# Optimization experiments

Hardware: AMD Instinct MI355X
Metric: run time of the kernel (lower is better)

Reference implementation:

```python
import jax, jax.numpy as jnp
import numpy as np

N_NODES = 100000
N_EDGES = 1600000
IN_DIM, HID, OUT_DIM = 128, 128, 64


def _glorot(key, fan_in, fan_out):
    s = float(np.sqrt(6.0 / (fan_in + fan_out)))
    return jax.random.uniform(key, (fan_in, fan_out), jnp.float32, -s, s)


def setup_inputs() -> dict:
    key = jax.random.key(0)
    ks = jax.random.split(key, 6)
    x = jax.random.normal(ks[0], (N_NODES, IN_DIM), jnp.float32)
    edge_index = jax.random.randint(ks[1], (2, N_EDGES), 0, N_NODES, jnp.int32)
    return {
        "x": x,
        "edge_index": edge_index,
        "W0": _glorot(ks[2], IN_DIM, HID), "b0": jnp.zeros((HID,), jnp.float32),
        "W1": _glorot(ks[3], HID, HID),    "b1": jnp.zeros((HID,), jnp.float32),
        "W2": _glorot(ks[4], HID, OUT_DIM), "b2": jnp.zeros((OUT_DIM,), jnp.float32),
    }


def _gcn_conv(x, src, dst, norm, W, b):
    # x' = D^{-1/2} (A+I) D^{-1/2} X W + b  (PyG GCNConv, add_self_loops=True)
    h = x @ W                       # [N, F_out]
    msg = h[src] * norm[:, None]    # [E+N, F_out] gathered, normalized messages
    out = jax.ops.segment_sum(msg, dst, num_segments=x.shape[0])
    return out + b


def reference(x, edge_index, W0, b0, W1, b1, W2, b2):
    n = x.shape[0]
    loop = jnp.arange(n, dtype=edge_index.dtype)
    src = jnp.concatenate([edge_index[0], loop])  # self-loops appended
    dst = jnp.concatenate([edge_index[1], loop])
    deg = jax.ops.segment_sum(jnp.ones_like(src, jnp.float32), dst, num_segments=n)
    dis = jnp.where(deg > 0, jax.lax.rsqrt(jnp.maximum(deg, 1e-12)), 0.0)
    norm = dis[src] * dis[dst]      # symmetric GCN normalization per edge

    h = jax.nn.relu(_gcn_conv(x, src, dst, norm, W0, b0))
    h = jax.nn.relu(_gcn_conv(h, src, dst, norm, W1, b1))
    h = jax.nn.relu(_gcn_conv(h, src, dst, norm, W2, b2))
    return jax.nn.log_softmax(h, axis=1)
```

## Files before the change

kernel.cpp:

```cpp
#include <hip/hip_runtime.h>

#define NN 100000
#define NE 1600000
#define NBK 782
#define NBLK 256
#define CHUNK ((NE + NBLK - 1) / NBLK)

typedef __bf16 bf16x4 __attribute__((ext_vector_type(4)));
typedef __bf16 bf16x8 __attribute__((ext_vector_type(8)));
typedef float f32x2 __attribute__((ext_vector_type(2)));
typedef float f32x4 __attribute__((ext_vector_type(4)));

#define ACC8_FP8(vv)                                                                  \
  {                                                                                   \
    f32x2 p;                                                                          \
    p = __builtin_amdgcn_cvt_pk_f32_fp8((vv).x, 0); acc[0] += p[0]; acc[1] += p[1];   \
    p = __builtin_amdgcn_cvt_pk_f32_fp8((vv).x, 1); acc[2] += p[0]; acc[3] += p[1];   \
    p = __builtin_amdgcn_cvt_pk_f32_fp8((vv).y, 0); acc[4] += p[0]; acc[5] += p[1];   \
    p = __builtin_amdgcn_cvt_pk_f32_fp8((vv).y, 1); acc[6] += p[0]; acc[7] += p[1];   \
  }


__global__ __launch_bounds__(256) void k1_hist(const int* __restrict__ dst, int* __restrict__ bhist,
                                               const float* __restrict__ W0, const float* __restrict__ W1,
                                               const float* __restrict__ W2, __bf16* __restrict__ Wt) {
  int b = blockIdx.x;
  if (b >= NBLK) {
    int i = (b - NBLK) * 256 + threadIdx.x;
    if (i < 16384) {
      int k = i >> 7, n = i & 127;
      Wt[n * 128 + k] = (__bf16)W0[i];
    } else if (i < 32768) {
      int j = i - 16384;
      int k = j >> 7, n = j & 127;
      Wt[16384 + n * 128 + k] = (__bf16)W1[j];
    } else if (i < 40960) {
      int j = i - 32768;
      int k = j >> 6, n = j & 63;
      Wt[32768 + n * 128 + k] = (__bf16)W2[j];
    }
    return;
  }
  __shared__ int h[NBK];
  int tid = threadIdx.x;
  for (int i = tid; i < NBK; i += 256) h[i] = 0;
  __syncthreads();
  int base = b * CHUNK, end = min(base + CHUNK, NE);
  for (int e = base + tid; e < end; e += 256) atomicAdd(&h[dst[e] >> 7], 1);
  __syncthreads();
  for (int i = tid; i < NBK; i += 256) bhist[i * NBLK + b] = h[i];
}

__global__ __launch_bounds__(256) void kA2(const int* __restrict__ bhist, int* __restrict__ btot) {
  int w = threadIdx.x >> 6, lane = threadIdx.x & 63;
  int bin = blockIdx.x * 4 + w;
  if (bin >= NBK) return;
  int4 v = *(const int4*)(bhist + bin * NBLK + lane * 4);
  int s = v.x + v.y + v.z + v.w;
#pragma unroll
  for (int off = 32; off > 0; off >>= 1) s += __shfl_xor(s, off);
  if (lane == 0) btot[bin] = s;
}

__global__ __launch_bounds__(1024) void kB_bscan(const int* __restrict__ btot, int* __restrict__ bptr) {
  __shared__ int ws[16];
  int tid = threadIdx.x, lane = tid & 63, w = tid >> 6;
  int v = (tid < NBK) ? btot[tid] : 0;
  int incl = v;
#pragma unroll
  for (int off = 1; off < 64; off <<= 1) {
    int t = __shfl_up(incl, off);
    if (lane >= off) incl += t;
  }
  if (lane == 63) ws[w] = incl;
  __syncthreads();
  if (tid < 16) {
    int s = ws[tid];
    int si = s;
#pragma unroll
    for (int off = 1; off < 16; off <<= 1) {
      int t = __shfl_up(si, off);
      if (lane >= off) si += t;
    }
    ws[tid] = si - s;
  }
  __syncthreads();
  if (tid < NBK) bptr[tid + 1] = incl + ws[w];
  if (tid == 0) bptr[0] = 0;
}

__global__ __launch_bounds__(256) void kC2(const int* __restrict__ bhist, const int* __restrict__ bptr,
                                           int* __restrict__ blockbase) {
  int w = threadIdx.x >> 6, lane = threadIdx.x & 63;
  int bin = blockIdx.x * 4 + w;
  if (bin >= NBK) return;
  int4 v = *(const int4*)(bhist + bin * NBLK + lane * 4);
  int ls = v.x + v.y + v.z + v.w;
  int incl = ls;
#pragma unroll
  for (int off = 1; off < 64; off <<= 1) {
    int t = __shfl_up(incl, off);
    if (lane >= off) incl += t;
  }
  int base = bptr[bin] + incl - ls;
  int4 o;
  o.x = base;
  o.y = base + v.x;
  o.z = base + v.x + v.y;
  o.w = base + v.x + v.y + v.z;
  *(int4*)(blockbase + bin * NBLK + lane * 4) = o;
}

__global__ __launch_bounds__(256) void k3_scatter(const int* __restrict__ src, const int* __restrict__ dst,
                                                  const int* __restrict__ blockbase, int* __restrict__ bucketed) {
  __shared__ int cur[NBK];
  int tid = threadIdx.x, b = blockIdx.x;
  for (int i = tid; i < NBK; i += 256) cur[i] = blockbase[i * NBLK + b];
  __syncthreads();
  int base = b * CHUNK, end = min(base + CHUNK, NE);
  for (int e = base + tid; e < end; e += 256) {
    int d = dst[e];
    int pos = atomicAdd(&cur[d >> 7], 1);
    bucketed[pos] = (src[e] << 7) | (d & 127);
  }
}

__global__ __launch_bounds__(256) void k_degfill(const int* __restrict__ bucketed, const int* __restrict__ bptr,
                                                 int* __restrict__ row_ptr, float* __restrict__ dis,
                                                 int* __restrict__ csr_src) {
  __shared__ int deg[128];
  __shared__ int sc[128];
  __shared__ int cur[128];
  int b = blockIdx.x, tid = threadIdx.x;
  int nb0 = b << 7;
  if (tid < 128) deg[tid] = 0;
  __syncthreads();
  int beg = bptr[b], end = bptr[b + 1];
  for (int e = beg + tid; e < end; e += 256) atomicAdd(&deg[bucketed[e] & 127], 1);
  __syncthreads();
  if (tid < 128) sc[tid] = deg[tid];
  __syncthreads();
  for (int off = 1; off < 128; off <<= 1) {
    int t = (tid >= off && tid < 128) ? sc[tid - off] : 0;
    __syncthreads();
    if (tid < 128) sc[tid] += t;
    __syncthreads();
  }
  if (tid < 128) {
    cur[tid] = beg + sc[tid] - deg[tid];
    if (nb0 + tid < NN) {
      row_ptr[nb0 + tid + 1] = beg + sc[tid];
      dis[nb0 + tid] = rsqrtf((float)(deg[tid] + 1));
      if (b == 0 && tid == 0) row_ptr[0] = 0;
    }
  }
  __syncthreads();
  for (int e = beg + tid; e < end; e += 256) {
    int pk = bucketed[e];
    int pos = atomicAdd(&cur[pk & 127], 1);
    csr_src[pos] = pk >> 7;
  }
}


template <int BN, int MODE, bool OUT8>
__global__ __launch_bounds__(512) void k_gemm(const void* __restrict__ Av, const __bf16* __restrict__ Wt,
                                              const float* __restrict__ bias, const float* __restrict__ dis,
                                              void* __restrict__ outv) {
  constexpr int LDK = 136;
  constexpr int NT = BN / 32;
  constexpr int ROWB = BN * (OUT8 ? 1 : 2);
  __shared__ __bf16 lB[BN * LDK];

  const int tid = threadIdx.x;
  const int rowBase = blockIdx.x * 128;
  const int lane = tid & 63;
  const int wid = tid >> 6;
  const int wm = (wid & 3) * 32;
  const int wn = (wid >> 2) * (BN / 2);
  const int lm = lane & 15;
  const int kg = lane >> 4;

  if (blockIdx.x == 0 && tid < ROWB / 16) {
    ((uint4*)((char*)outv + (size_t)NN * ROWB))[tid] = make_uint4(0, 0, 0, 0);
  }

  for (int c = tid; c < 16 * BN; c += 512) {
    int n = c >> 4;
    int koff = (c & 15) * 8;
    bf16x8 w = *(const bf16x8*)(Wt + n * 128 + koff);
    *(bf16x8*)&lB[n * LDK + koff] = w;
  }
  __syncthreads();

  f32x4 acc[2][NT] = {};
  const bool full = (rowBase + 128 <= NN);

#pragma unroll 2
  for (int ks = 0; ks < 128; ks += 32) {
    int k0 = ks + kg * 8;
    bf16x8 af[2];
    if constexpr (MODE == 0) {
      const float* A = (const float*)Av;
#pragma unroll
      for (int tm = 0; tm < 2; ++tm) {
        int gr = rowBase + wm + tm * 16 + lm;
        f32x4 a0 = {}, a1 = {};
        if (full || gr < NN) {
          a0 = *(const f32x4*)(A + (size_t)gr * 128 + k0);
          a1 = *(const f32x4*)(A + (size_t)gr * 128 + k0 + 4);
        }
        af[tm] = bf16x8{(__bf16)a0[0], (__bf16)a0[1], (__bf16)a0[2], (__bf16)a0[3],
                        (__bf16)a1[0], (__bf16)a1[1], (__bf16)a1[2], (__bf16)a1[3]};
      }
    } else {
      const __bf16* A = (const __bf16*)Av;
      f32x4 b0 = *(const f32x4*)(bias + k0);
      f32x4 b1 = *(const f32x4*)(bias + k0 + 4);
#pragma unroll
      for (int tm = 0; tm < 2; ++tm) {
        int gr = rowBase + wm + tm * 16 + lm;
        bf16x8 v = {};
        if (full || gr < NN) v = *(const bf16x8*)(A + (size_t)gr * 128 + k0);
        af[tm] = bf16x8{(__bf16)fmaxf((float)v[0] + b0[0], 0.f), (__bf16)fmaxf((float)v[1] + b0[1], 0.f),
                        (__bf16)fmaxf((float)v[2] + b0[2], 0.f), (__bf16)fmaxf((float)v[3] + b0[3], 0.f),
                        (__bf16)fmaxf((float)v[4] + b1[0], 0.f), (__bf16)fmaxf((float)v[5] + b1[1], 0.f),
                        (__bf16)fmaxf((float)v[6] + b1[2], 0.f), (__bf16)fmaxf((float)v[7] + b1[3], 0.f)};
      }
    }
    bf16x8 bfr[NT];
#pragma unroll
    for (int tn = 0; tn < NT; ++tn)
      bfr[tn] = *(const bf16x8*)&lB[(wn + tn * 16 + lm) * LDK + k0];
#pragma unroll
    for (int tm = 0; tm < 2; ++tm)
#pragma unroll
      for (int tn = 0; tn < NT; ++tn)
        acc[tm][tn] = __builtin_amdgcn_mfma_f32_16x16x32_bf16(af[tm], bfr[tn], acc[tm][tn], 0, 0, 0);
  }

#pragma unroll
  for (int tm = 0; tm < 2; ++tm) {
    int r0 = rowBase + wm + tm * 16 + kg * 4;
#pragma unroll
    for (int tn = 0; tn < NT; ++tn) {
      int c0 = wn + tn * 16 + lm;
#pragma unroll
      for (int r = 0; r < 4; ++r) {
        int gr = r0 + r;
        if (full || gr < NN) {
          float val = acc[tm][tn][r] * dis[gr];
          if constexpr (OUT8) {
            unsigned char* o8 = (unsigned char*)outv;
            unsigned pk = __builtin_amdgcn_cvt_pk_fp8_f32(val, val, 0, 0);
            o8[(size_t)gr * BN + c0] = (unsigned char)(pk & 0xffu);
          } else {
            __bf16* ob = (__bf16*)outv;
            ob[(size_t)gr * BN + c0] = (__bf16)val;
          }
        }
      }
    }
  }
}


__global__ __launch_bounds__(256) void k_agg128(const unsigned char* __restrict__ tmp8, const int* __restrict__ row_ptr,
                                                const int* __restrict__ csr_src, const float* __restrict__ dis,
                                                __bf16* __restrict__ agg) {
  int qw = (blockIdx.x * 256 + threadIdx.x) >> 6;
  int lane = threadIdx.x & 63;
  int g = lane >> 4;
  int fl = lane & 15;
  int node = qw * 4 + g;

  int beg = row_ptr[node];
  int end = row_ptr[node + 1];

  int mx = end - beg;
  mx = max(mx, __shfl_xor(mx, 16));
  mx = max(mx, __shfl_xor(mx, 32));

  float acc[8] = {};
  {
    uint2 sv = *(const uint2*)(tmp8 + (size_t)node * 128 + fl * 8);
    ACC8_FP8(sv);
  }

  for (int done = 0; done < mx; done += 16) {
    int ep = beg + done + fl;
    int sidx = (ep < end) ? csr_src[ep] : NN;
    int rem = mx - done;
    {
      uint2 v[8];
#pragma unroll
      for (int u = 0; u < 8; ++u) {
        int s = __shfl(sidx, g * 16 + u);
        v[u] = *(const uint2*)(tmp8 + (size_t)s * 128 + fl * 8);
      }
#pragma unroll
      for (int u = 0; u < 8; ++u) ACC8_FP8(v[u]);
    }
    if (rem > 8) {
      uint2 v[8];
#pragma unroll
      for (int u = 0; u < 8; ++u) {
        int s = __shfl(sidx, g * 16 + 8 + u);
        v[u] = *(const uint2*)(tmp8 + (size_t)s * 128 + fl * 8);
      }
#pragma unroll
      for (int u = 0; u < 8; ++u) ACC8_FP8(v[u]);
    }
  }

  float d = dis[node];
  bf16x8 o;
#pragma unroll
  for (int t = 0; t < 8; ++t) o[t] = (__bf16)(acc[t] * d);
  *(bf16x8*)&agg[(size_t)node * 128 + fl * 8] = o;
}


__global__ __launch_bounds__(256) void k_agg64_final(const __bf16* __restrict__ tmp, const int* __restrict__ row_ptr,
                                                     const int* __restrict__ csr_src, const float* __restrict__ dis,
                                                     const float* __restrict__ b2, float* __restrict__ out) {
  int qw = (blockIdx.x * 256 + threadIdx.x) >> 6;
  int lane = threadIdx.x & 63;
  int g = lane >> 4;
  int fl = lane & 15;
  int node = qw * 4 + g;

  int beg = row_ptr[node];
  int end = row_ptr[node + 1];

  int mx = end - beg;
  mx = max(mx, __shfl_xor(mx, 16));
  mx = max(mx, __shfl_xor(mx, 32));

  float acc[4] = {};
  {
    bf16x4 sv = *(const bf16x4*)&tmp[(size_t)node * 64 + fl * 4];
#pragma unroll
    for (int t = 0; t < 4; ++t) acc[t] = (float)sv[t];
  }

  for (int done = 0; done < mx; done += 16) {
    int ep = beg + done + fl;
    int sidx = (ep < end) ? csr_src[ep] : NN;
    int rem = mx - done;
    {
      bf16x4 v[8];
#pragma unroll
      for (int u = 0; u < 8; ++u) {
        int s = __shfl(sidx, g * 16 + u);
        v[u] = *(const bf16x4*)&tmp[(size_t)s * 64 + fl * 4];
      }
#pragma unroll
      for (int u = 0; u < 8; ++u)
#pragma unroll
        for (int t = 0; t < 4; ++t) acc[t] += (float)v[u][t];
    }
    if (rem > 8) {
      bf16x4 v[8];
#pragma unroll
      for (int u = 0; u < 8; ++u) {
        int s = __shfl(sidx, g * 16 + 8 + u);
        v[u] = *(const bf16x4*)&tmp[(size_t)s * 64 + fl * 4];
      }
#pragma unroll
      for (int u = 0; u < 8; ++u)
#pragma unroll
        for (int t = 0; t < 4; ++t) acc[t] += (float)v[u][t];
    }
  }

  float d = dis[node];
  float v4[4], lm = -1e30f;
#pragma unroll
  for (int t = 0; t < 4; ++t) {
    v4[t] = fmaxf(acc[t] * d + b2[fl * 4 + t], 0.f);
    lm = fmaxf(lm, v4[t]);
  }
#pragma unroll
  for (int off = 8; off > 0; off >>= 1) lm = fmaxf(lm, __shfl_xor(lm, off));
  float le = 0.f;
#pragma unroll
  for (int t = 0; t < 4; ++t) le += __expf(v4[t] - lm);
#pragma unroll
  for (int off = 8; off > 0; off >>= 1) le += __shfl_xor(le, off);
  float ls = lm + __logf(le);
  f32x4 o = {v4[0] - ls, v4[1] - ls, v4[2] - ls, v4[3] - ls};
  *(f32x4*)&out[(size_t)node * 64 + fl * 4] = o;
}


extern "C" void kernel_launch(void* const* d_in, const int* in_sizes, int n_in,
                              void* d_out, int out_size, void* d_ws, size_t ws_size,
                              hipStream_t stream) {
  const float* x  = (const float*)d_in[0];
  const int*   ei = (const int*)d_in[1];
  const float* W0 = (const float*)d_in[2];
  const float* b0 = (const float*)d_in[3];
  const float* W1 = (const float*)d_in[4];
  const float* b1 = (const float*)d_in[5];
  const float* W2 = (const float*)d_in[6];
  const float* b2 = (const float*)d_in[7];
  const int* esrc = ei;
  const int* edst = ei + NE;

  char* p = (char*)d_ws;
  auto alloc = [&](size_t bytes) {
    char* q = p;
    p += (bytes + 255) & ~(size_t)255;
    return q;
  };
  float*  dis     = (float*)alloc((size_t)NN * 4);
  int*    row_ptr = (int*)alloc((size_t)(NN + 1) * 4);
  int*    btot    = (int*)alloc(NBK * 4);
  int*    bptr    = (int*)alloc((NBK + 1) * 4);
  __bf16* Wt      = (__bf16*)alloc(40960 * 2);
  int*    csr_src = (int*)alloc((size_t)NE * 4);
  char*   tmp     = (char*)alloc((size_t)(NN + 1) * 128 * 2);
  unsigned char* tmp8 = (unsigned char*)tmp;
  __bf16* tmp16   = (__bf16*)tmp;
  int*    bucketed  = (int*)tmp;
  int*    bhist     = csr_src;
  int*    blockbase = csr_src + NBLK * NBK;

  k1_hist<<<NBLK + 160, 256, 0, stream>>>(edst, bhist, W0, W1, W2, Wt);
  kA2<<<(NBK + 3) / 4, 256, 0, stream>>>(bhist, btot);
  kB_bscan<<<1, 1024, 0, stream>>>(btot, bptr);
  kC2<<<(NBK + 3) / 4, 256, 0, stream>>>(bhist, bptr, blockbase);
  k3_scatter<<<NBLK, 256, 0, stream>>>(esrc, edst, blockbase, bucketed);
  k_degfill<<<NBK, 256, 0, stream>>>(bucketed, bptr, row_ptr, dis, csr_src);

  int gblocks = (NN + 127) / 128;
  int ablocks = NN / 16;

  k_gemm<128, 0, true><<<gblocks, 512, 0, stream>>>(x, Wt, nullptr, dis, tmp8);
  k_agg128<<<ablocks, 256, 0, stream>>>(tmp8, row_ptr, csr_src, dis, (__bf16*)d_out);

  k_gemm<128, 2, true><<<gblocks, 512, 0, stream>>>(d_out, Wt + 16384, b0, dis, tmp8);
  k_agg128<<<ablocks, 256, 0, stream>>>(tmp8, row_ptr, csr_src, dis, (__bf16*)d_out);

  k_gemm<64, 2, false><<<gblocks, 512, 0, stream>>>(d_out, Wt + 32768, b1, dis, tmp16);
  k_agg64_final<<<ablocks, 256, 0, stream>>>(tmp16, row_ptr, csr_src, dis, b2, (float*)d_out);
}
```

Baseline: 319.9 us.

## Make GEMM kernels persistent over row tiles and preload full A rows

New measurement: 339.5 us. 1.06x slower.

```diff
diff --git a/kernel.cpp b/kernel.cpp
--- a/kernel.cpp
+++ b/kernel.cpp
@@ -170,10 +170,10 @@
   constexpr int LDK = 136;
   constexpr int NT = BN / 32;
   constexpr int ROWB = BN * (OUT8 ? 1 : 2);
+  constexpr int NTILE = (NN + 127) / 128;
   __shared__ __bf16 lB[BN * LDK];
 
   const int tid = threadIdx.x;
-  const int rowBase = blockIdx.x * 128;
   const int lane = tid & 63;
   const int wid = tid >> 6;
   const int wm = (wid & 3) * 32;
@@ -188,75 +188,92 @@
   for (int c = tid; c < 16 * BN; c += 512) {
     int n = c >> 4;
     int koff = (c & 15) * 8;
-    bf16x8 w = *(const bf16x8*)(Wt + n * 128 + koff);
-    *(bf16x8*)&lB[n * LDK + koff] = w;
-  }
-  __syncthreads();
-
-  f32x4 acc[2][NT] = {};
-  const bool full = (rowBase + 128 <= NN);
-
-#pragma unroll 2
-  for (int ks = 0; ks < 128; ks += 32) {
-    int k0 = ks + kg * 8;
-    bf16x8 af[2];
-    if constexpr (MODE == 0) {
-      const float* A = (const float*)Av;
+    *(bf16x8*)&lB[n * LDK + koff] = *(const bf16x8*)(Wt + n * 128 + koff);
+  }
+  __syncthreads();
+
+  for (int tile = blockIdx.x; tile < NTILE; tile += 256) {
+    const int rowBase = tile * 128;
+    const bool full = (rowBase + 128 <= NN);
+
+    f32x4 a0[4][2], a1[4][2];
+    bf16x8 araw[4][2];
+#pragma unroll
+    for (int ks4 = 0; ks4 < 4; ++ks4) {
+      int k0 = ks4 * 32 + kg * 8;
 #pragma unroll
       for (int tm = 0; tm < 2; ++tm) {
         int gr = rowBase + wm + tm * 16 + lm;
-        f32x4 a0 = {}, a1 = {};
-        if (full || gr < NN) {
-          a0 = *(const f32x4*)(A + (size_t)gr * 128 + k0);
-          a1 = *(const f32x4*)(A + (size_t)gr * 128 + k0 + 4);
+        if constexpr (MODE == 0) {
+          const float* A = (const float*)Av;
+          a0[ks4][tm] = f32x4{};
+          a1[ks4][tm] = f32x4{};
+          if (full || gr < NN) {
+            a0[ks4][tm] = *(const f32x4*)(A + (size_t)gr * 128 + k0);
+            a1[ks4][tm] = *(const f32x4*)(A + (size_t)gr * 128 + k0 + 4);
+          }
+        } else {
+          const __bf16* A = (const __bf16*)Av;
+          araw[ks4][tm] = bf16x8{};
+          if (full || gr < NN) araw[ks4][tm] = *(const bf16x8*)(A + (size_t)gr * 128 + k0);
         }
-        af[tm] = bf16x8{(__bf16)a0[0], (__bf16)a0[1], (__bf16)a0[2], (__bf16)a0[3],
-                        (__bf16)a1[0], (__bf16)a1[1], (__bf16)a1[2], (__bf16)a1[3]};
-      }
-    } else {
-      const __bf16* A = (const __bf16*)Av;
-      f32x4 b0 = *(const f32x4*)(bias + k0);
-      f32x4 b1 = *(const f32x4*)(bias + k0 + 4);
-#pragma unroll
-      for (int tm = 0; tm < 2; ++tm) {
-        int gr = rowBase + wm + tm * 16 + lm;
-        bf16x8 v = {};
-        if (full || gr < NN) v = *(const bf16x8*)(A + (size_t)gr * 128 + k0);
-        af[tm] = bf16x8{(__bf16)fmaxf((float)v[0] + b0[0], 0.f), (__bf16)fmaxf((float)v[1] + b0[1], 0.f),
-                        (__bf16)fmaxf((float)v[2] + b0[2], 0.f), (__bf16)fmaxf((float)v[3] + b0[3], 0.f),
-                        (__bf16)fmaxf((float)v[4] + b1[0], 0.f), (__bf16)fmaxf((float)v[5] + b1[1], 0.f),
-                        (__bf16)fmaxf((float)v[6] + b1[2], 0.f), (__bf16)fmaxf((float)v[7] + b1[3], 0.f)};
-      }
-    }
-    bf16x8 bfr[NT];
-#pragma unroll
-    for (int tn = 0; tn < NT; ++tn)
-      bfr[tn] = *(const bf16x8*)&lB[(wn + tn * 16 + lm) * LDK + k0];
-#pragma unroll
-    for (int tm = 0; tm < 2; ++tm)
+      }
+    }
+
+    f32x4 acc[2][NT] = {};
+#pragma unroll
+    for (int ks4 = 0; ks4 < 4; ++ks4) {
+      int k0 = ks4 * 32 + kg * 8;
+      bf16x8 af[2];
+      if constexpr (MODE == 0) {
+#pragma unroll
+        for (int tm = 0; tm < 2; ++tm) {
+          f32x4 A0 = a0[ks4][tm], A1 = a1[ks4][tm];
+          af[tm] = bf16x8{(__bf16)A0[0], (__bf16)A0[1], (__bf16)A0[2], (__bf16)A0[3],
+                          (__bf16)A1[0], (__bf16)A1[1], (__bf16)A1[2], (__bf16)A1[3]};
+        }
+      } else {
+        f32x4 b0 = *(const f32x4*)(bias + k0);
+        f32x4 b1 = *(const f32x4*)(bias + k0 + 4);
+#pragma unroll
+        for (int tm = 0; tm < 2; ++tm) {
+          bf16x8 v = araw[ks4][tm];
+          af[tm] = bf16x8{(__bf16)fmaxf((float)v[0] + b0[0], 0.f), (__bf16)fmaxf((float)v[1] + b0[1], 0.f),
+                          (__bf16)fmaxf((float)v[2] + b0[2], 0.f), (__bf16)fmaxf((float)v[3] + b0[3], 0.f),
+                          (__bf16)fmaxf((float)v[4] + b1[0], 0.f), (__bf16)fmaxf((float)v[5] + b1[1], 0.f),
+                          (__bf16)fmaxf((float)v[6] + b1[2], 0.f), (__bf16)fmaxf((float)v[7] + b1[3], 0.f)};
+        }
+      }
+      bf16x8 bfr[NT];
 #pragma unroll
       for (int tn = 0; tn < NT; ++tn)
-        acc[tm][tn] = __builtin_amdgcn_mfma_f32_16x16x32_bf16(af[tm], bfr[tn], acc[tm][tn], 0, 0, 0);
-  }
-
-#pragma unroll
-  for (int tm = 0; tm < 2; ++tm) {
-    int r0 = rowBase + wm + tm * 16 + kg * 4;
-#pragma unroll
-    for (int tn = 0; tn < NT; ++tn) {
-      int c0 = wn + tn * 16 + lm;
-#pragma unroll
-      for (int r = 0; r < 4; ++r) {
-        int gr = r0 + r;
-        if (full || gr < NN) {
-          float val = acc[tm][tn][r] * dis[gr];
-          if constexpr (OUT8) {
-            unsigned char* o8 = (unsigned char*)outv;
-            unsigned pk = __builtin_amdgcn_cvt_pk_fp8_f32(val, val, 0, 0);
-            o8[(size_t)gr * BN + c0] = (unsigned char)(pk & 0xffu);
-          } else {
-            __bf16* ob = (__bf16*)outv;
-            ob[(size_t)gr * BN + c0] = (__bf16)val;
+        bfr[tn] = *(const bf16x8*)&lB[(wn + tn * 16 + lm) * LDK + k0];
+#pragma unroll
+      for (int tm = 0; tm < 2; ++tm)
+#pragma unroll
+        for (int tn = 0; tn < NT; ++tn)
+          acc[tm][tn] = __builtin_amdgcn_mfma_f32_16x16x32_bf16(af[tm], bfr[tn], acc[tm][tn], 0, 0, 0);
+    }
+
+#pragma unroll
+    for (int tm = 0; tm < 2; ++tm) {
+      int r0 = rowBase + wm + tm * 16 + kg * 4;
+#pragma unroll
+      for (int tn = 0; tn < NT; ++tn) {
+        int c0 = wn + tn * 16 + lm;
+#pragma unroll
+        for (int r = 0; r < 4; ++r) {
+          int gr = r0 + r;
+          if (full || gr < NN) {
+            float val = acc[tm][tn][r] * dis[gr];
+            if constexpr (OUT8) {
+              unsigned char* o8 = (unsigned char*)outv;
+              unsigned pk = __builtin_amdgcn_cvt_pk_fp8_f32(val, val, 0, 0);
+              o8[(size_t)gr * BN + c0] = (unsigned char)(pk & 0xffu);
+            } else {
+              __bf16* ob = (__bf16*)outv;
+              ob[(size_t)gr * BN + c0] = (__bf16)val;
+            }
           }
         }
       }
@@ -434,15 +451,14 @@
   k3_scatter<<<NBLK, 256, 0, stream>>>(esrc, edst, blockbase, bucketed);
   k_degfill<<<NBK, 256, 0, stream>>>(bucketed, bptr, row_ptr, dis, csr_src);
 
-  int gblocks = (NN + 127) / 128;
   int ablocks = NN / 16;
 
-  k_gemm<128, 0, true><<<gblocks, 512, 0, stream>>>(x, Wt, nullptr, dis, tmp8);
+  k_gemm<128, 0, true><<<256, 512, 0, stream>>>(x, Wt, nullptr, dis, tmp8);
   k_agg128<<<ablocks, 256, 0, stream>>>(tmp8, row_ptr, csr_src, dis, (__bf16*)d_out);
 
-  k_gemm<128, 2, true><<<gblocks, 512, 0, stream>>>(d_out, Wt + 16384, b0, dis, tmp8);
+  k_gemm<128, 2, true><<<256, 512, 0, stream>>>(d_out, Wt + 16384, b0, dis, tmp8);
   k_agg128<<<ablocks, 256, 0, stream>>>(tmp8, row_ptr, csr_src, dis, (__bf16*)d_out);
 
-  k_gemm<64, 2, false><<<gblocks, 512, 0, stream>>>(d_out, Wt + 32768, b1, dis, tmp16);
+  k_gemm<64, 2, false><<<256, 512, 0, stream>>>(d_out, Wt + 32768, b1, dis, tmp16);
   k_agg64_final<<<ablocks, 256, 0, stream>>>(tmp16, row_ptr, csr_src, dis, b2, (float*)d_out);
 }
```

## Compute degrees early and overlap first GEMM with CSR scatter and fill

Applied to the files above, without the earlier changes.

New measurement: 373.2 us. 16.6% more time.

```diff
diff --git a/kernel.cpp b/kernel.cpp
--- a/kernel.cpp
+++ b/kernel.cpp
@@ -5,6 +5,7 @@
 #define NBK 782
 #define NBLK 256
 #define CHUNK ((NE + NBLK - 1) / NBLK)
+#define G0H 391
 
 typedef __bf16 bf16x4 __attribute__((ext_vector_type(4)));
 typedef __bf16 bf16x8 __attribute__((ext_vector_type(8)));
@@ -23,7 +24,8 @@
 
 __global__ __launch_bounds__(256) void k1_hist(const int* __restrict__ dst, int* __restrict__ bhist,
                                                const float* __restrict__ W0, const float* __restrict__ W1,
-                                               const float* __restrict__ W2, __bf16* __restrict__ Wt) {
+                                               const float* __restrict__ W2, __bf16* __restrict__ Wt,
+                                               int* __restrict__ deg) {
   int b = blockIdx.x;
   if (b >= NBLK) {
     int i = (b - NBLK) * 256 + threadIdx.x;
@@ -46,14 +48,25 @@
   for (int i = tid; i < NBK; i += 256) h[i] = 0;
   __syncthreads();
   int base = b * CHUNK, end = min(base + CHUNK, NE);
-  for (int e = base + tid; e < end; e += 256) atomicAdd(&h[dst[e] >> 7], 1);
+  for (int e = base + tid; e < end; e += 256) {
+    int d = dst[e];
+    atomicAdd(&h[d >> 7], 1);
+    atomicAdd(&deg[d], 1);
+  }
   __syncthreads();
   for (int i = tid; i < NBK; i += 256) bhist[i * NBLK + b] = h[i];
 }
 
-__global__ __launch_bounds__(256) void kA2(const int* __restrict__ bhist, int* __restrict__ btot) {
+__global__ __launch_bounds__(256) void kA2(const int* __restrict__ bhist, int* __restrict__ btot,
+                                           const int* __restrict__ deg, float* __restrict__ dis) {
+  int b = blockIdx.x;
+  if (b >= (NBK + 3) / 4) {
+    int i = (b - (NBK + 3) / 4) * 256 + threadIdx.x;
+    if (i < NN) dis[i] = rsqrtf((float)(deg[i] + 1));
+    return;
+  }
   int w = threadIdx.x >> 6, lane = threadIdx.x & 63;
-  int bin = blockIdx.x * 4 + w;
+  int bin = b * 4 + w;
   if (bin >= NBK) return;
   int4 v = *(const int4*)(bhist + bin * NBLK + lane * 4);
   int s = v.x + v.y + v.z + v.w;
@@ -111,69 +124,17 @@
   *(int4*)(blockbase + bin * NBLK + lane * 4) = o;
 }
 
-__global__ __launch_bounds__(256) void k3_scatter(const int* __restrict__ src, const int* __restrict__ dst,
-                                                  const int* __restrict__ blockbase, int* __restrict__ bucketed) {
-  __shared__ int cur[NBK];
-  int tid = threadIdx.x, b = blockIdx.x;
-  for (int i = tid; i < NBK; i += 256) cur[i] = blockbase[i * NBLK + b];
-  __syncthreads();
-  int base = b * CHUNK, end = min(base + CHUNK, NE);
-  for (int e = base + tid; e < end; e += 256) {
-    int d = dst[e];
-    int pos = atomicAdd(&cur[d >> 7], 1);
-    bucketed[pos] = (src[e] << 7) | (d & 127);
-  }
-}
-
-__global__ __launch_bounds__(256) void k_degfill(const int* __restrict__ bucketed, const int* __restrict__ bptr,
-                                                 int* __restrict__ row_ptr, float* __restrict__ dis,
-                                                 int* __restrict__ csr_src) {
-  __shared__ int deg[128];
-  __shared__ int sc[128];
-  __shared__ int cur[128];
-  int b = blockIdx.x, tid = threadIdx.x;
-  int nb0 = b << 7;
-  if (tid < 128) deg[tid] = 0;
-  __syncthreads();
-  int beg = bptr[b], end = bptr[b + 1];
-  for (int e = beg + tid; e < end; e += 256) atomicAdd(&deg[bucketed[e] & 127], 1);
-  __syncthreads();
-  if (tid < 128) sc[tid] = deg[tid];
-  __syncthreads();
-  for (int off = 1; off < 128; off <<= 1) {
-    int t = (tid >= off && tid < 128) ? sc[tid - off] : 0;
-    __syncthreads();
-    if (tid < 128) sc[tid] += t;
-    __syncthreads();
-  }
-  if (tid < 128) {
-    cur[tid] = beg + sc[tid] - deg[tid];
-    if (nb0 + tid < NN) {
-      row_ptr[nb0 + tid + 1] = beg + sc[tid];
-      dis[nb0 + tid] = rsqrtf((float)(deg[tid] + 1));
-      if (b == 0 && tid == 0) row_ptr[0] = 0;
-    }
-  }
-  __syncthreads();
-  for (int e = beg + tid; e < end; e += 256) {
-    int pk = bucketed[e];
-    int pos = atomicAdd(&cur[pk & 127], 1);
-    csr_src[pos] = pk >> 7;
-  }
-}
-
 
 template <int BN, int MODE, bool OUT8>
-__global__ __launch_bounds__(512) void k_gemm(const void* __restrict__ Av, const __bf16* __restrict__ Wt,
-                                              const float* __restrict__ bias, const float* __restrict__ dis,
-                                              void* __restrict__ outv) {
+__device__ __forceinline__ void gemm_tile(const void* __restrict__ Av, const __bf16* __restrict__ Wt,
+                                          const float* __restrict__ bias, const float* __restrict__ dis,
+                                          void* __restrict__ outv, int tile, __bf16* lB) {
   constexpr int LDK = 136;
   constexpr int NT = BN / 32;
   constexpr int ROWB = BN * (OUT8 ? 1 : 2);
-  __shared__ __bf16 lB[BN * LDK];
 
   const int tid = threadIdx.x;
-  const int rowBase = blockIdx.x * 128;
+  const int rowBase = tile * 128;
   const int lane = tid & 63;
   const int wid = tid >> 6;
   const int wm = (wid & 3) * 32;
@@ -181,15 +142,14 @@
   const int lm = lane & 15;
   const int kg = lane >> 4;
 
-  if (blockIdx.x == 0 && tid < ROWB / 16) {
+  if (tile == 0 && tid < ROWB / 16) {
     ((uint4*)((char*)outv + (size_t)NN * ROWB))[tid] = make_uint4(0, 0, 0, 0);
   }
 
   for (int c = tid; c < 16 * BN; c += 512) {
     int n = c >> 4;
     int koff = (c & 15) * 8;
-    bf16x8 w = *(const bf16x8*)(Wt + n * 128 + koff);
-    *(bf16x8*)&lB[n * LDK + koff] = w;
+    *(bf16x8*)&lB[n * LDK + koff] = *(const bf16x8*)(Wt + n * 128 + koff);
   }
   __syncthreads();
 
@@ -265,6 +225,82 @@
 }
 
 
+__global__ __launch_bounds__(512) void k_scat_g0(const int* __restrict__ src, const int* __restrict__ dst,
+                                                 const int* __restrict__ blockbase, int* __restrict__ bucketed,
+                                                 const float* __restrict__ x, const __bf16* __restrict__ Wt,
+                                                 const float* __restrict__ dis, unsigned char* __restrict__ tmp8) {
+  __shared__ __bf16 smem[128 * 136];
+  int b = blockIdx.x;
+  if (b < NBLK) {
+    int* cur = (int*)smem;
+    int tid = threadIdx.x;
+    for (int i = tid; i < NBK; i += 512) cur[i] = blockbase[i * NBLK + b];
+    __syncthreads();
+    int base = b * CHUNK, end = min(base + CHUNK, NE);
+    for (int e = base + tid; e < end; e += 512) {
+      int d = dst[e];
+      int pos = atomicAdd(&cur[d >> 7], 1);
+      bucketed[pos] = (src[e] << 7) | (d & 127);
+    }
+    return;
+  }
+  gemm_tile<128, 0, true>(x, Wt, nullptr, dis, tmp8, b - NBLK, smem);
+}
+
+
+__global__ __launch_bounds__(512) void k_degf_g0(const int* __restrict__ bucketed, const int* __restrict__ bptr,
+                                                 int* __restrict__ row_ptr, int* __restrict__ csr_src,
+                                                 const float* __restrict__ x, const __bf16* __restrict__ Wt,
+                                                 const float* __restrict__ dis, unsigned char* __restrict__ tmp8) {
+  __shared__ __bf16 smem[128 * 136];
+  int b = blockIdx.x;
+  if (b < NBK) {
+    int* deg_s = (int*)smem;
+    int* sc = deg_s + 128;
+    int* cur = sc + 128;
+    int tid = threadIdx.x;
+    int nb0 = b << 7;
+    if (tid < 128) deg_s[tid] = 0;
+    __syncthreads();
+    int beg = bptr[b], end = bptr[b + 1];
+    for (int e = beg + tid; e < end; e += 512) atomicAdd(&deg_s[bucketed[e] & 127], 1);
+    __syncthreads();
+    if (tid < 128) sc[tid] = deg_s[tid];
+    __syncthreads();
+    for (int off = 1; off < 128; off <<= 1) {
+      int t = (tid >= off && tid < 128) ? sc[tid - off] : 0;
+      __syncthreads();
+      if (tid < 128) sc[tid] += t;
+      __syncthreads();
+    }
+    if (tid < 128) {
+      cur[tid] = beg + sc[tid] - deg_s[tid];
+      if (nb0 + tid < NN) {
+        row_ptr[nb0 + tid + 1] = beg + sc[tid];
+        if (b == 0 && tid == 0) row_ptr[0] = 0;
+      }
+    }
+    __syncthreads();
+    for (int e = beg + tid; e < end; e += 512) {
+      int pk = bucketed[e];
+      int pos = atomicAdd(&cur[pk & 127], 1);
+      csr_src[pos] = pk >> 7;
+    }
+    return;
+  }
+  gemm_tile<128, 0, true>(x, Wt, nullptr, dis, tmp8, G0H + (b - NBK), smem);
+}
+
+
+template <int BN, int MODE, bool OUT8>
+__global__ __launch_bounds__(512) void k_gemm(const void* __restrict__ Av, const __bf16* __restrict__ Wt,
+                                              const float* __restrict__ bias, const float* __restrict__ dis,
+                                              void* __restrict__ outv) {
+  __shared__ __bf16 lB[BN * 136];
+  gemm_tile<BN, MODE, OUT8>(Av, Wt, bias, dis, outv, blockIdx.x, lB);
+}
+
+
 __global__ __launch_bounds__(256) void k_agg128(const unsigned char* __restrict__ tmp8, const int* __restrict__ row_ptr,
                                                 const int* __restrict__ csr_src, const float* __restrict__ dis,
                                                 __bf16* __restrict__ agg) {
@@ -418,26 +454,29 @@
   int*    row_ptr = (int*)alloc((size_t)(NN + 1) * 4);
   int*    btot    = (int*)alloc(NBK * 4);
   int*    bptr    = (int*)alloc((NBK + 1) * 4);
+  int*    deg     = (int*)alloc((size_t)NN * 4);
   __bf16* Wt      = (__bf16*)alloc(40960 * 2);
   int*    csr_src = (int*)alloc((size_t)NE * 4);
+  int*    bucketed= (int*)alloc((size_t)NE * 4);
   char*   tmp     = (char*)alloc((size_t)(NN + 1) * 128 * 2);
   unsigned char* tmp8 = (unsigned char*)tmp;
   __bf16* tmp16   = (__bf16*)tmp;
-  int*    bucketed  = (int*)tmp;
   int*    bhist     = csr_src;
   int*    blockbase = csr_src + NBLK * NBK;
 
-  k1_hist<<<NBLK + 160, 256, 0, stream>>>(edst, bhist, W0, W1, W2, Wt);
-  kA2<<<(NBK + 3) / 4, 256, 0, stream>>>(bhist, btot);
+  hipMemsetAsync(deg, 0, (size_t)NN * 4, stream);
+
+  k1_hist<<<NBLK + 160, 256, 0, stream>>>(edst, bhist, W0, W1, W2, Wt, deg);
+  kA2<<<(NBK + 3) / 4 + (NN + 255) / 256, 256, 0, stream>>>(bhist, btot, deg, dis);
   kB_bscan<<<1, 1024, 0, stream>>>(btot, bptr);
   kC2<<<(NBK + 3) / 4, 256, 0, stream>>>(bhist, bptr, blockbase);
-  k3_scatter<<<NBLK, 256, 0, stream>>>(esrc, edst, blockbase, bucketed);
-  k_degfill<<<NBK, 256, 0, stream>>>(bucketed, bptr, row_ptr, dis, csr_src);
-
+
+  k_scat_g0<<<NBLK + G0H, 512, 0, stream>>>(esrc, edst, blockbase, bucketed, x, Wt, dis, tmp8);
+  k_degf_g0<<<NBK + G0H, 512, 0, stream>>>(bucketed, bptr, row_ptr, csr_src, x, Wt, dis, tmp8);
+
+  int ablocks = NN / 16;
   int gblocks = (NN + 127) / 128;
-  int ablocks = NN / 16;
-
-  k_gemm<128, 0, true><<<gblocks, 512, 0, stream>>>(x, Wt, nullptr, dis, tmp8);
+
   k_agg128<<<ablocks, 256, 0, stream>>>(tmp8, row_ptr, csr_src, dis, (__bf16*)d_out);
 
   k_gemm<128, 2, true><<<gblocks, 512, 0, stream>>>(d_out, Wt + 16384, b0, dis, tmp8);
```
